# Performance work log

Hardware: AMD Instinct MI355X
Metric: run time of the kernel (lower is better)

## Reference

```python
import jax, jax.numpy as jnp
import numpy as np

DIM = 768
HEADS = 12
HD = DIM // HEADS  # 64
WIN = 14
N = WIN * WIN  # 196
MLP_HID = 3072
EPS = 1e-6
SCALE = HD ** -0.5


def _ln(x, g, b):
    m = jnp.mean(x, axis=-1, keepdims=True)
    v = jnp.mean(jnp.square(x - m), axis=-1, keepdims=True)
    return (x - m) * jax.lax.rsqrt(v + EPS) * g + b


def _rel_table(rel):
    coords = jnp.arange(WIN)[:, None] - jnp.arange(WIN)[None, :] + (WIN - 1)
    return rel[coords]


def _window_partition(x, ws):
    B, H, W, C = x.shape
    pad_h = (ws - H % ws) % ws
    pad_w = (ws - W % ws) % ws
    x = jnp.pad(x, ((0, 0), (0, pad_h), (0, pad_w), (0, 0)))
    Hp, Wp = H + pad_h, W + pad_w
    x = x.reshape(B, Hp // ws, ws, Wp // ws, ws, C)
    win = x.transpose(0, 1, 3, 2, 4, 5).reshape(-1, ws, ws, C)
    return win, (Hp, Wp)


def _window_unpartition(win, ws, pad_hw, hw):
    Hp, Wp = pad_hw
    H, W = hw
    B = win.shape[0] // (Hp * Wp // ws // ws)
    x = win.reshape(B, Hp // ws, Wp // ws, ws, ws, -1)
    x = x.transpose(0, 1, 3, 2, 4, 5).reshape(B, Hp, Wp, -1)
    return x[:, :H, :W, :]


def _attention(x, qkv_w, qkv_b, proj_w, proj_b, rel_pos_h, rel_pos_w):
    Bw = x.shape[0]
    qkv = x.reshape(Bw, N, DIM) @ qkv_w + qkv_b  # (Bw, N, 3*DIM)
    qkv = qkv.reshape(Bw, N, 3, HEADS, HD).transpose(2, 0, 3, 1, 4)
    qkv = qkv.reshape(3, Bw * HEADS, N, HD)
    q, k, v = qkv[0], qkv[1], qkv[2]
    attn = jnp.einsum('bnd,bmd->bnm', q * SCALE, k)  # (Bw*H, N, N)
    Rh = _rel_table(rel_pos_h)
    Rw = _rel_table(rel_pos_w)
    r_q = q.reshape(-1, WIN, WIN, HD)
    rel_h = jnp.einsum('bhwc,hkc->bhwk', r_q, Rh)
    rel_w = jnp.einsum('bhwc,wkc->bhwk', r_q, Rw)
    attn = (attn.reshape(-1, WIN, WIN, WIN, WIN)
            + rel_h[:, :, :, :, None]
            + rel_w[:, :, :, None, :]).reshape(-1, N, N)
    attn = jax.nn.softmax(attn, axis=-1)
    out = jnp.einsum('bnm,bmd->bnd', attn, v)
    out = out.reshape(Bw, HEADS, WIN, WIN, HD).transpose(0, 2, 3, 1, 4)
    out = out.reshape(Bw, WIN, WIN, DIM)
    return out @ proj_w + proj_b


def setup_inputs() -> dict:
    key = jax.random.key(0)
    ks = jax.random.split(key, 10)
    s = 0.02
    return {
        'x': jax.random.normal(ks[0], (2, 64, 64, DIM), jnp.float32),
        'ln1_g': jnp.ones((DIM,), jnp.float32),
        'ln1_b': jnp.zeros((DIM,), jnp.float32),
        'qkv_w': jax.random.normal(ks[1], (DIM, 3 * DIM), jnp.float32) * s,
        'qkv_b': jax.random.normal(ks[2], (3 * DIM,), jnp.float32) * s,
        'proj_w': jax.random.normal(ks[3], (DIM, DIM), jnp.float32) * s,
        'proj_b': jax.random.normal(ks[4], (DIM,), jnp.float32) * s,
        'rel_pos_h': jax.random.normal(ks[5], (2 * WIN - 1, HD), jnp.float32) * s,
        'rel_pos_w': jax.random.normal(ks[6], (2 * WIN - 1, HD), jnp.float32) * s,
        'ln2_g': jnp.ones((DIM,), jnp.float32),
        'ln2_b': jnp.zeros((DIM,), jnp.float32),
        'fc1_w': jax.random.normal(ks[7], (DIM, MLP_HID), jnp.float32) * s,
        'fc1_b': jnp.zeros((MLP_HID,), jnp.float32),
        'fc2_w': jax.random.normal(ks[8], (MLP_HID, DIM), jnp.float32) * s,
        'fc2_b': jnp.zeros((DIM,), jnp.float32),
    }


def reference(x, ln1_g, ln1_b, qkv_w, qkv_b, proj_w, proj_b,
              rel_pos_h, rel_pos_w, ln2_g, ln2_b, fc1_w, fc1_b, fc2_w, fc2_b):
    B, H, W, _ = x.shape
    shortcut = x
    h = _ln(x, ln1_g, ln1_b)
    win, pad_hw = _window_partition(h, WIN)
    win = _attention(win, qkv_w, qkv_b, proj_w, proj_b, rel_pos_h, rel_pos_w)
    h = _window_unpartition(win, WIN, pad_hw, (H, W))
    x = shortcut + h  # drop_path prob 0 -> identity
    h = _ln(x, ln2_g, ln2_b)
    h = jax.nn.gelu(h @ fc1_w + fc1_b, approximate=False) @ fc2_w + fc2_b
    return x + h
```

## Files before the change

kernel.cpp:

```cpp
#include <hip/hip_runtime.h>
#include <hip/hip_bf16.h>
#include <math.h>


#define DIMC 768
#define HEADS 12
#define WIN 14
#define NTOK 196
#define NWIN 50
#define MROWS 9800
#define YROWS 8192
#define MLP_HID 3072

using bf16x8 = __attribute__((ext_vector_type(8))) short;
using f32x4  = __attribute__((ext_vector_type(4))) float;

__device__ __forceinline__ float bf2f(unsigned short u) {
    return __uint_as_float(((unsigned)u) << 16);
}
__device__ __forceinline__ unsigned short f2bf(float f) {
    unsigned u = __float_as_uint(f);
    unsigned r = (u + 0x7fffu + ((u >> 16) & 1u)) >> 16;
    return (unsigned short)r;
}
__device__ __forceinline__ void gl2lds16(const unsigned short* g, unsigned short* l) {
    __builtin_amdgcn_global_load_lds(
        (const __attribute__((address_space(1))) void*)g,
        (__attribute__((address_space(3))) void*)l, 16, 0, 0);
}

__global__ __launch_bounds__(256) void transpose_w(
        const float* __restrict__ W, unsigned short* __restrict__ Wt,
        int K, int N) {
    __shared__ float t[64][65];
    int k0 = blockIdx.y << 6, n0 = blockIdx.x << 6;
    int tn = threadIdx.x & 63;
    int tk = threadIdx.x >> 6;
    #pragma unroll
    for (int r = 0; r < 16; r++) {
        int k = tk + r * 4;
        t[k][tn] = W[(size_t)(k0 + k) * N + n0 + tn];
    }
    __syncthreads();
    #pragma unroll
    for (int r = 0; r < 16; r++) {
        int n = tk + r * 4;
        Wt[(size_t)(n0 + n) * K + k0 + tn] = f2bf(t[tn][n]);
    }
}

__global__ __launch_bounds__(256) void ln1_win_kernel(
        const float* __restrict__ x, const float* __restrict__ g,
        const float* __restrict__ b, unsigned short* __restrict__ h1) {
    int tid = threadIdx.x;
    int row = blockIdx.x * 4 + (tid >> 6);
    int lane = tid & 63;
    if (row >= MROWS) return;
    int w = row / NTOK, t = row % NTOK;
    int bi = w / 25, wr = w % 25;
    int gy = (wr / 5) * WIN + t / WIN;
    int gx = (wr % 5) * WIN + t % WIN;
    unsigned short* out = h1 + (size_t)row * DIMC;
    if (gy >= 64 || gx >= 64) {
        #pragma unroll
        for (int j = 0; j < 12; j++) out[lane + 64 * j] = 0;
        return;
    }
    const float* xr = x + ((size_t)((bi * 64 + gy) * 64 + gx)) * DIMC;
    float v[12], s = 0.f;
    #pragma unroll
    for (int j = 0; j < 12; j++) { v[j] = xr[lane + 64 * j]; s += v[j]; }
    #pragma unroll
    for (int o = 32; o > 0; o >>= 1) s += __shfl_xor(s, o);
    float mean = s * (1.f / 768.f);
    float q = 0.f;
    #pragma unroll
    for (int j = 0; j < 12; j++) { float d = v[j] - mean; q += d * d; }
    #pragma unroll
    for (int o = 32; o > 0; o >>= 1) q += __shfl_xor(q, o);
    float inv = rsqrtf(q * (1.f / 768.f) + 1e-6f);
    #pragma unroll
    for (int j = 0; j < 12; j++) {
        int c = lane + 64 * j;
        out[c] = f2bf((v[j] - mean) * inv * g[c] + b[c]);
    }
}

__global__ __launch_bounds__(256) void ln2_kernel(
        const float* __restrict__ y, const float* __restrict__ g,
        const float* __restrict__ b, unsigned short* __restrict__ h2) {
    int tid = threadIdx.x;
    int row = blockIdx.x * 4 + (tid >> 6);
    int lane = tid & 63;
    const float* xr = y + (size_t)row * DIMC;
    float v[12], s = 0.f;
    #pragma unroll
    for (int j = 0; j < 12; j++) { v[j] = xr[lane + 64 * j]; s += v[j]; }
    #pragma unroll
    for (int o = 32; o > 0; o >>= 1) s += __shfl_xor(s, o);
    float mean = s * (1.f / 768.f);
    float q = 0.f;
    #pragma unroll
    for (int j = 0; j < 12; j++) { float d = v[j] - mean; q += d * d; }
    #pragma unroll
    for (int o = 32; o > 0; o >>= 1) q += __shfl_xor(q, o);
    float inv = rsqrtf(q * (1.f / 768.f) + 1e-6f);
    unsigned short* out = h2 + (size_t)row * DIMC;
    #pragma unroll
    for (int j = 0; j < 12; j++) {
        int c = lane + 64 * j;
        out[c] = f2bf((v[j] - mean) * inv * g[c] + b[c]);
    }
}

__global__ __launch_bounds__(256) void build_aug(
        const unsigned short* __restrict__ qkvb,
        const float* __restrict__ relph, const float* __restrict__ relpw,
        unsigned short* __restrict__ Aaug, unsigned short* __restrict__ Vt) {
    __shared__ unsigned short qs[208 * 72];
    __shared__ unsigned short rt[64 * 72];
    int tid = threadIdx.x;
    int bh = blockIdx.x, w = bh / HEADS, head = bh % HEADS;
    int lane = tid & 63, wave = tid >> 6;
    int l15 = lane & 15, q4 = lane >> 4, q8 = q4 * 8;
    size_t base = (size_t)w * NTOK * 2304 + head * 64;
    unsigned short* ab = Aaug + (size_t)bh * 256 * 96;

    for (int e = tid; e < 196 * 8; e += 256) {
        int t = e >> 3, s8 = (e & 7) * 8;
        bf16x8 qv = *(const bf16x8*)&qkvb[base + (size_t)t * 2304 + s8];
        *(bf16x8*)&qs[t * 72 + s8] = qv;
        *(bf16x8*)&ab[t * 96 + s8] = qv;
    }
    for (int e = tid; e < 12 * 8; e += 256) {
        bf16x8 z = {};
        *(bf16x8*)&qs[(196 + (e >> 3)) * 72 + (e & 7) * 8] = z;
    }
    for (int e = tid; e < 64 * 8; e += 256) {
        int r = e >> 3, s8 = (e & 7) * 8;
        bf16x8 ov = {};
        if (r < 54) {
            const float* src = (r < 27 ? relph + (size_t)r * 64
                                       : relpw + (size_t)(r - 27) * 64) + s8;
            #pragma unroll
            for (int jj = 0; jj < 8; jj++) ov[jj] = (short)f2bf(src[jj]);
        }
        *(bf16x8*)&rt[r * 72 + s8] = ov;
    }
    for (int e = tid; e < 60 * 12; e += 256) {
        bf16x8 z = {};
        *(bf16x8*)&ab[(size_t)(196 + e / 12) * 96 + (e % 12) * 8] = z;
    }
    for (int e = tid; e < 196; e += 256) {
        ab[e * 96 + 92] = 0; ab[e * 96 + 93] = 0;
        ab[e * 96 + 94] = 0; ab[e * 96 + 95] = 0;
    }
    __syncthreads();

    #pragma unroll
    for (int t = 0; t < 4; t++) {
        int it = wave * 4 + t;
        if (it >= 13) break;
        bf16x8 a0 = *(bf16x8*)&qs[(it * 16 + l15) * 72 + q8];
        bf16x8 a1 = *(bf16x8*)&qs[(it * 16 + l15) * 72 + 32 + q8];
        #pragma unroll
        for (int rt4 = 0; rt4 < 4; rt4++) {
            bf16x8 b0 = *(bf16x8*)&rt[(rt4 * 16 + l15) * 72 + q8];
            bf16x8 b1 = *(bf16x8*)&rt[(rt4 * 16 + l15) * 72 + 32 + q8];
            f32x4 d4 = {};
            d4 = __builtin_amdgcn_mfma_f32_16x16x32_bf16(a0, b0, d4, 0, 0, 0);
            d4 = __builtin_amdgcn_mfma_f32_16x16x32_bf16(a1, b1, d4, 0, 0, 0);
            int rcol = rt4 * 16 + l15;
            #pragma unroll
            for (int r = 0; r < 4; r++) {
                int i = it * 16 + q4 * 4 + r;
                if (i < 196 && rcol < 54) {
                    if (rcol < 27) {
                        int c = 13 + i / 14 - rcol;
                        if (c >= 0 && c < 14) ab[i * 96 + 64 + c] = f2bf(d4[r]);
                    } else {
                        int c = 13 + i % 14 - (rcol - 27);
                        if (c >= 0 && c < 14) ab[i * 96 + 78 + c] = f2bf(d4[r]);
                    }
                }
            }
        }
    }

    unsigned short* vtb = Vt + (size_t)bh * 64 * 224;
    for (int e = tid; e < 196 * 8; e += 256) {
        int j = e >> 3, dg = (e & 7) * 8;
        bf16x8 vv = *(const bf16x8*)&qkvb[base + 1536 + (size_t)j * 2304 + dg];
        #pragma unroll
        for (int k = 0; k < 8; k++)
            vtb[(size_t)(dg + k) * 224 + j] = (unsigned short)vv[k];
    }
    for (int e = tid; e < 64 * 28; e += 256)
        vtb[(size_t)(e / 28) * 224 + 196 + (e % 28)] = 0;
}

__global__ __launch_bounds__(256) void attn_mfma(
        const unsigned short* __restrict__ qkvb,
        const unsigned short* __restrict__ Aaug,
        const unsigned short* __restrict__ Vt,
        unsigned short* __restrict__ out) {
    __shared__ unsigned short Kls[208 * 96];
    __shared__ unsigned short Pls[4][64 * 40];
    int tid = threadIdx.x;
    int bh = blockIdx.x, w = bh / HEADS, head = bh % HEADS;
    int wave = tid >> 6, lane = tid & 63;
    int l15 = lane & 15, q4 = lane >> 4, q8 = q4 * 8;
    size_t kbase = (size_t)w * NTOK * 2304 + head * 64 + 768;
    for (int e = tid; e < 196 * 8; e += 256) {
        int t = e >> 3, s8 = (e & 7) * 8;
        bf16x8 kv = *(const bf16x8*)&qkvb[kbase + (size_t)t * 2304 + s8];
        bf16x8 ko;
        #pragma unroll
        for (int jj = 0; jj < 8; jj++)
            ko[jj] = (short)f2bf(bf2f((unsigned short)kv[jj]) * 0.125f);
        *(bf16x8*)&Kls[t * 96 + s8] = ko;
    }
    bf16x8 z8 = {};
    for (int e = tid; e < 208 * 4; e += 256)
        *(bf16x8*)&Kls[(e >> 2) * 96 + 64 + (e & 3) * 8] = z8;
    for (int e = tid; e < 12 * 8; e += 256)
        *(bf16x8*)&Kls[(196 + (e >> 3)) * 96 + (e & 7) * 8] = z8;
    __syncthreads();
    for (int e = tid; e < 196; e += 256) {
        Kls[e * 96 + 64 + e / WIN] = 0x3F80;
        Kls[e * 96 + 78 + e % WIN] = 0x3F80;
    }
    bf16x8 af[4][3];
    const unsigned short* abse = Aaug + (size_t)bh * 256 * 96;
    #pragma unroll
    for (int it = 0; it < 4; it++)
        #pragma unroll
        for (int c = 0; c < 3; c++)
            af[it][c] = *(const bf16x8*)&abse[(size_t)(wave * 64 + it * 16 + l15) * 96 + c * 32 + q8];
    __syncthreads();

    const unsigned short* vtb = Vt + (size_t)bh * 64 * 224;
    f32x4 o[4][4] = {};
    float lacc[4][4] = {{0.f}};
    bf16x8 bv[4];
    #pragma unroll
    for (int dt = 0; dt < 4; dt++)
        bv[dt] = *(const bf16x8*)&vtb[(dt * 16 + l15) * 224 + q8];

    for (int jp = 0; jp < 7; jp++) {
        f32x4 s[4][2] = {};
        #pragma unroll
        for (int half = 0; half < 2; half++) {
            int jt = jp * 2 + half;
            if (jt < 13) {
                #pragma unroll
                for (int c = 0; c < 3; c++) {
                    bf16x8 bk = *(bf16x8*)&Kls[(jt * 16 + l15) * 96 + c * 32 + q8];
                    #pragma unroll
                    for (int it = 0; it < 4; it++)
                        s[it][half] = __builtin_amdgcn_mfma_f32_16x16x32_bf16(
                            af[it][c], bk, s[it][half], 0, 0, 0);
                }
            }
        }
        __syncthreads();
        #pragma unroll
        for (int half = 0; half < 2; half++) {
            int jt = jp * 2 + half;
            bool valid = (jt < 13) && (jt * 16 + l15) < 196;
            #pragma unroll
            for (int it = 0; it < 4; it++)
                #pragma unroll
                for (int r = 0; r < 4; r++) {
                    float p = valid ? __expf(s[it][half][r]) : 0.f;
                    unsigned short pb = f2bf(p);
                    lacc[it][r] += bf2f(pb);
                    Pls[wave][(it * 16 + q4 * 4 + r) * 40 + half * 16 + l15] = pb;
                }
        }
        __syncthreads();
        bf16x8 ap[4];
        #pragma unroll
        for (int it = 0; it < 4; it++)
            ap[it] = *(bf16x8*)&Pls[wave][(it * 16 + l15) * 40 + q8];
        bf16x8 bvn[4];
        if (jp < 6) {
            #pragma unroll
            for (int dt = 0; dt < 4; dt++)
                bvn[dt] = *(const bf16x8*)&vtb[(dt * 16 + l15) * 224 + (jp + 1) * 32 + q8];
        }
        #pragma unroll
        for (int dt = 0; dt < 4; dt++)
            #pragma unroll
            for (int it = 0; it < 4; it++)
                o[it][dt] = __builtin_amdgcn_mfma_f32_16x16x32_bf16(
                    ap[it], bv[dt], o[it][dt], 0, 0, 0);
        if (jp < 6) {
            #pragma unroll
            for (int dt = 0; dt < 4; dt++) bv[dt] = bvn[dt];
        }
    }
    #pragma unroll
    for (int it = 0; it < 4; it++)
        #pragma unroll
        for (int r = 0; r < 4; r++) {
            float v = lacc[it][r];
            v += __shfl_xor(v, 1); v += __shfl_xor(v, 2);
            v += __shfl_xor(v, 4); v += __shfl_xor(v, 8);
            lacc[it][r] = 1.f / v;
        }
    #pragma unroll
    for (int it = 0; it < 4; it++) {
        int i0 = wave * 64 + it * 16 + q4 * 4;
        #pragma unroll
        for (int r = 0; r < 4; r++) {
            if (i0 + r < 196) {
                size_t rowb = (size_t)(w * NTOK + i0 + r) * DIMC + head * 64;
                #pragma unroll
                for (int dt = 0; dt < 4; dt++)
                    out[rowb + dt * 16 + l15] = f2bf(o[it][dt][r] * lacc[it][r]);
            }
        }
    }
}

template <int EPI, int BN>
__global__ __launch_bounds__(256) void mgemm(
        const unsigned short* __restrict__ A, const unsigned short* __restrict__ Bt,
        const float* __restrict__ bias, void* __restrict__ Cout,
        const float* __restrict__ resid, int M, int Nn, int K,
        int nbx, int nby) {
    const int NI = BN / 32;
    __shared__ unsigned short As[128 * 32];
    __shared__ unsigned short Bs[BN * 32];
    int tid = threadIdx.x;
    int lane = tid & 63, wave = tid >> 6;
    int l15 = lane & 15, q4 = lane >> 4;
    int xq8 = (q4 ^ ((l15 >> 1) & 3)) * 8;
    int id = blockIdx.x;
    int per = nbx * 8;
    int s = id / per;
    int rem = id - s * per;
    int rmax = nby - s * 8; if (rmax > 8) rmax = 8;
    int bx = rem / rmax;
    int r_ = rem - bx * rmax;
    int by = s * 8 + r_;
    int m0 = by << 7, n0 = bx * BN;
    int wm = (wave >> 1) * 64, wn = (wave & 1) * (BN / 2);
    int srow0 = wave * 32 + (lane >> 2);
    int srow1 = srow0 + 16;
    int sseg = ((lane & 3) ^ ((lane >> 3) & 3)) * 8;
    int rmA0 = m0 + srow0; if (rmA0 >= M) rmA0 = M - 1;
    int rmA1 = m0 + srow1; if (rmA1 >= M) rmA1 = M - 1;
    const unsigned short* gA0 = A + (size_t)rmA0 * K + sseg;
    const unsigned short* gA1 = A + (size_t)rmA1 * K + sseg;
    unsigned short* lA0 = As + wave * 1024 + lane * 8;
    unsigned short* lA1 = lA0 + 512;
    int browB = (BN == 128) ? srow0 : (wave * 16 + (lane >> 2));
    const unsigned short* gB0 = Bt + (size_t)(n0 + browB) * K + sseg;
    const unsigned short* gB1 = Bt + (size_t)(n0 + srow1) * K + sseg;
    unsigned short* lB0 = Bs + ((BN == 128) ? wave * 1024 : wave * 512) + lane * 8;
    unsigned short* lB1 = lB0 + 512;
    f32x4 acc[4][NI] = {};
    for (int k0 = 0; k0 < K; k0 += 32) {
        gl2lds16(gA0 + k0, lA0);
        gl2lds16(gA1 + k0, lA1);
        gl2lds16(gB0 + k0, lB0);
        if (BN == 128) gl2lds16(gB1 + k0, lB1);
        __syncthreads();
        bf16x8 bfr[NI];
        #pragma unroll
        for (int ni = 0; ni < NI; ni++)
            bfr[ni] = *(bf16x8*)&Bs[(wn + ni * 16 + l15) * 32 + xq8];
        #pragma unroll
        for (int mi = 0; mi < 4; mi++) {
            bf16x8 afr = *(bf16x8*)&As[(wm + mi * 16 + l15) * 32 + xq8];
            #pragma unroll
            for (int ni = 0; ni < NI; ni++)
                acc[mi][ni] = __builtin_amdgcn_mfma_f32_16x16x32_bf16(
                    afr, bfr[ni], acc[mi][ni], 0, 0, 0);
        }
        __syncthreads();
    }
    int q4r = (lane >> 4) * 4;
    #pragma unroll
    for (int mi = 0; mi < 4; mi++) {
        #pragma unroll
        for (int r = 0; r < 4; r++) {
            int row = m0 + wm + mi * 16 + q4r + r;
            if (row >= M) continue;
            if (EPI == 2) {
                int w = row / NTOK, t = row % NTOK;
                int bi = w / 25, wr = w % 25;
                int gy = (wr / 5) * WIN + t / WIN;
                int gx = (wr % 5) * WIN + t % WIN;
                if (gy >= 64 || gx >= 64) continue;
                size_t orow = ((size_t)((bi * 64 + gy) * 64 + gx)) * DIMC;
                #pragma unroll
                for (int ni = 0; ni < NI; ni++) {
                    int col = n0 + wn + ni * 16 + l15;
                    float v = acc[mi][ni][r] + bias[col];
                    ((float*)Cout)[orow + col] = resid[orow + col] + v;
                }
            } else {
                #pragma unroll
                for (int ni = 0; ni < NI; ni++) {
                    int col = n0 + wn + ni * 16 + l15;
                    float v = acc[mi][ni][r] + bias[col];
                    if (EPI == 0) {
                        ((unsigned short*)Cout)[(size_t)row * Nn + col] = f2bf(v);
                    } else if (EPI == 1) {
                        v = 0.5f * v * (1.f + erff(v * 0.70710678118654752f));
                        ((unsigned short*)Cout)[(size_t)row * Nn + col] = f2bf(v);
                    } else {
                        ((float*)Cout)[(size_t)row * Nn + col] =
                            resid[(size_t)row * Nn + col] + v;
                    }
                }
            }
        }
    }
}

extern "C" void kernel_launch(void* const* d_in, const int* in_sizes, int n_in,
                              void* d_out, int out_size, void* d_ws, size_t ws_size,
                              hipStream_t stream) {
    const float* x      = (const float*)d_in[0];
    const float* ln1_g  = (const float*)d_in[1];
    const float* ln1_b  = (const float*)d_in[2];
    const float* qkv_w  = (const float*)d_in[3];
    const float* qkv_b  = (const float*)d_in[4];
    const float* proj_w = (const float*)d_in[5];
    const float* proj_b = (const float*)d_in[6];
    const float* rel_h  = (const float*)d_in[7];
    const float* rel_w  = (const float*)d_in[8];
    const float* ln2_g  = (const float*)d_in[9];
    const float* ln2_b  = (const float*)d_in[10];
    const float* fc1_w  = (const float*)d_in[11];
    const float* fc1_b  = (const float*)d_in[12];
    const float* fc2_w  = (const float*)d_in[13];
    const float* fc2_b  = (const float*)d_in[14];
    float* out = (float*)d_out;
    char* ws = (char*)d_ws;

    unsigned short* wt_qkv  = (unsigned short*)(ws);
    unsigned short* wt_proj = (unsigned short*)(ws + 3538944);
    unsigned short* wt_fc1  = (unsigned short*)(ws + 4718592);
    unsigned short* wt_fc2  = (unsigned short*)(ws + 9437184);
    unsigned short* qkvb    = (unsigned short*)(ws + 14155776);
    float*          yb      = (float*)        (ws + 14155776);
    unsigned short* h2      = (unsigned short*)(ws + 39321600);
    unsigned short* h1      = (unsigned short*)(ws + 59314176);
    unsigned short* attn_o  = h1;
    unsigned short* zb      = h1;
    unsigned short* Aaug    = (unsigned short*)(ws + 74366976);
    unsigned short* Vt      = (unsigned short*)(ws + 103858176);

    transpose_w<<<dim3(36, 12), 256, 0, stream>>>(qkv_w,  wt_qkv,  768, 2304);
    transpose_w<<<dim3(12, 12), 256, 0, stream>>>(proj_w, wt_proj, 768, 768);
    transpose_w<<<dim3(48, 12), 256, 0, stream>>>(fc1_w,  wt_fc1,  768, 3072);
    transpose_w<<<dim3(12, 48), 256, 0, stream>>>(fc2_w,  wt_fc2,  3072, 768);

    ln1_win_kernel<<<(MROWS + 3) / 4, 256, 0, stream>>>(x, ln1_g, ln1_b, h1);

    mgemm<0, 128><<<18 * 77, 256, 0, stream>>>(
        h1, wt_qkv, qkv_b, qkvb, nullptr, MROWS, 2304, DIMC, 18, 77);

    build_aug<<<NWIN * HEADS, 256, 0, stream>>>(qkvb, rel_h, rel_w, Aaug, Vt);

    attn_mfma<<<NWIN * HEADS, 256, 0, stream>>>(qkvb, Aaug, Vt, attn_o);

    mgemm<2, 64><<<12 * 77, 256, 0, stream>>>(
        attn_o, wt_proj, proj_b, yb, x, MROWS, DIMC, DIMC, 12, 77);

    ln2_kernel<<<YROWS / 4, 256, 0, stream>>>(yb, ln2_g, ln2_b, h2);

    mgemm<1, 128><<<24 * 64, 256, 0, stream>>>(
        h2, wt_fc1, fc1_b, zb, nullptr, YROWS, MLP_HID, DIMC, 24, 64);

    mgemm<3, 64><<<12 * 64, 256, 0, stream>>>(
        zb, wt_fc2, fc2_b, out, yb, YROWS, DIMC, MLP_HID, 12, 64);
}
```

Before: 448.4 us.

## Double-buffer GEMM LDS tiles and merge weight transposes into one launch

The mgemm main loop now keeps two LDS buffers per operand. It prefetches the next K-slice with global_load_lds right after the barrier, then runs MFMAs on the current slice, so one barrier per iteration replaces two. The four weight-transpose launches are merged into a single kernel that picks its matrix from the block index, removing launch overhead. The cost is doubled LDS per block, which may lower occupancy. The overlap also depends on the compiler not forcing a full vmcnt wait before the LDS reads.

Result: no change. 442.5 us (-1.3%).

```diff
diff --git a/kernel.cpp b/kernel.cpp
--- a/kernel.cpp
+++ b/kernel.cpp
@@ -29,11 +29,20 @@
         (__attribute__((address_space(3))) void*)l, 16, 0, 0);
 }
 
-__global__ __launch_bounds__(256) void transpose_w(
-        const float* __restrict__ W, unsigned short* __restrict__ Wt,
-        int K, int N) {
+__global__ __launch_bounds__(256) void transpose_all(
+        const float* __restrict__ Wq, unsigned short* __restrict__ Tq,
+        const float* __restrict__ Wp, unsigned short* __restrict__ Tp,
+        const float* __restrict__ W1, unsigned short* __restrict__ T1,
+        const float* __restrict__ W2, unsigned short* __restrict__ T2) {
+    int id = blockIdx.x;
+    const float* W; unsigned short* Wt; int K, N, nbx, rel;
+    if (id < 432)       { W = Wq; Wt = Tq; K = 768;  N = 2304; nbx = 36; rel = id; }
+    else if (id < 576)  { W = Wp; Wt = Tp; K = 768;  N = 768;  nbx = 12; rel = id - 432; }
+    else if (id < 1152) { W = W1; Wt = T1; K = 768;  N = 3072; nbx = 48; rel = id - 576; }
+    else                { W = W2; Wt = T2; K = 3072; N = 768;  nbx = 12; rel = id - 1152; }
+    int bx = rel % nbx, by = rel / nbx;
     __shared__ float t[64][65];
-    int k0 = blockIdx.y << 6, n0 = blockIdx.x << 6;
+    int k0 = by << 6, n0 = bx << 6;
     int tn = threadIdx.x & 63;
     int tk = threadIdx.x >> 6;
     #pragma unroll
@@ -331,8 +340,8 @@
         const float* __restrict__ resid, int M, int Nn, int K,
         int nbx, int nby) {
     const int NI = BN / 32;
-    __shared__ unsigned short As[128 * 32];
-    __shared__ unsigned short Bs[BN * 32];
+    __shared__ unsigned short As[2][128 * 32];
+    __shared__ unsigned short Bs[2][BN * 32];
     int tid = threadIdx.x;
     int lane = tid & 63, wave = tid >> 6;
     int l15 = lane & 15, q4 = lane >> 4;
@@ -354,33 +363,39 @@
     int rmA1 = m0 + srow1; if (rmA1 >= M) rmA1 = M - 1;
     const unsigned short* gA0 = A + (size_t)rmA0 * K + sseg;
     const unsigned short* gA1 = A + (size_t)rmA1 * K + sseg;
-    unsigned short* lA0 = As + wave * 1024 + lane * 8;
-    unsigned short* lA1 = lA0 + 512;
     int browB = (BN == 128) ? srow0 : (wave * 16 + (lane >> 2));
     const unsigned short* gB0 = Bt + (size_t)(n0 + browB) * K + sseg;
     const unsigned short* gB1 = Bt + (size_t)(n0 + srow1) * K + sseg;
-    unsigned short* lB0 = Bs + ((BN == 128) ? wave * 1024 : wave * 512) + lane * 8;
-    unsigned short* lB1 = lB0 + 512;
+    int lofsA = wave * 1024 + lane * 8;
+    int lofsB = ((BN == 128) ? wave * 1024 : wave * 512) + lane * 8;
     f32x4 acc[4][NI] = {};
+    gl2lds16(gA0, &As[0][lofsA]);
+    gl2lds16(gA1, &As[0][lofsA + 512]);
+    gl2lds16(gB0, &Bs[0][lofsB]);
+    if (BN == 128) gl2lds16(gB1, &Bs[0][lofsB + 512]);
+    int cur = 0;
     for (int k0 = 0; k0 < K; k0 += 32) {
-        gl2lds16(gA0 + k0, lA0);
-        gl2lds16(gA1 + k0, lA1);
-        gl2lds16(gB0 + k0, lB0);
-        if (BN == 128) gl2lds16(gB1 + k0, lB1);
         __syncthreads();
+        int kn = k0 + 32;
+        if (kn < K) {
+            gl2lds16(gA0 + kn, &As[cur ^ 1][lofsA]);
+            gl2lds16(gA1 + kn, &As[cur ^ 1][lofsA + 512]);
+            gl2lds16(gB0 + kn, &Bs[cur ^ 1][lofsB]);
+            if (BN == 128) gl2lds16(gB1 + kn, &Bs[cur ^ 1][lofsB + 512]);
+        }
         bf16x8 bfr[NI];
         #pragma unroll
         for (int ni = 0; ni < NI; ni++)
-            bfr[ni] = *(bf16x8*)&Bs[(wn + ni * 16 + l15) * 32 + xq8];
+            bfr[ni] = *(bf16x8*)&Bs[cur][(wn + ni * 16 + l15) * 32 + xq8];
         #pragma unroll
         for (int mi = 0; mi < 4; mi++) {
-            bf16x8 afr = *(bf16x8*)&As[(wm + mi * 16 + l15) * 32 + xq8];
+            bf16x8 afr = *(bf16x8*)&As[cur][(wm + mi * 16 + l15) * 32 + xq8];
             #pragma unroll
             for (int ni = 0; ni < NI; ni++)
                 acc[mi][ni] = __builtin_amdgcn_mfma_f32_16x16x32_bf16(
                     afr, bfr[ni], acc[mi][ni], 0, 0, 0);
         }
-        __syncthreads();
+        cur ^= 1;
     }
     int q4r = (lane >> 4) * 4;
     #pragma unroll
@@ -456,10 +471,8 @@
     unsigned short* Aaug    = (unsigned short*)(ws + 74366976);
     unsigned short* Vt      = (unsigned short*)(ws + 103858176);
 
-    transpose_w<<<dim3(36, 12), 256, 0, stream>>>(qkv_w,  wt_qkv,  768, 2304);
-    transpose_w<<<dim3(12, 12), 256, 0, stream>>>(proj_w, wt_proj, 768, 768);
-    transpose_w<<<dim3(48, 12), 256, 0, stream>>>(fc1_w,  wt_fc1,  768, 3072);
-    transpose_w<<<dim3(12, 48), 256, 0, stream>>>(fc2_w,  wt_fc2,  3072, 768);
+    transpose_all<<<1728, 256, 0, stream>>>(
+        qkv_w, wt_qkv, proj_w, wt_proj, fc1_w, wt_fc1, fc2_w, wt_fc2);
 
     ln1_win_kernel<<<(MROWS + 3) / 4, 256, 0, stream>>>(x, ln1_g, ln1_b, h1);
 
```
